# Performance work log

Hardware: AMD Instinct MI355X
Metric: run time of the kernel (lower is better)

The kernel has to match this reference:

```python
import jax, jax.numpy as jnp
import numpy as np

N, D, T = 4096, 256, 32
GAMMA = 1.0 / 256.0  # 1/d
ALPHA = 1.0


def _rbf_kernel(X, Y, gamma):
    # K[i, j] = exp(-gamma * ||X[i] - Y[j]||^2), vectorized (replaces the
    # original per-(i,j) Python double loop).
    x2 = jnp.sum(X * X, axis=1)  # [n]
    y2 = jnp.sum(Y * Y, axis=1)  # [m]
    d2 = x2[:, None] + y2[None, :] - 2.0 * (X @ Y.T)  # [n, m]
    d2 = jnp.maximum(d2, 0.0)  # numerical guard; exact form is non-negative
    return jnp.exp(-gamma * d2)


def setup_inputs() -> dict:
    key = jax.random.key(0)
    kx, ky = jax.random.split(key)
    X = jax.random.normal(kx, (N, D), dtype=jnp.float32)
    y = jax.random.normal(ky, (N, T), dtype=jnp.float32)
    return {"X": X, "y": y}


def reference(X, y):
    # fit: K = rbf(X, X); dual = solve(K + alpha*I, y)
    K = _rbf_kernel(X, X, GAMMA)  # [N, N]
    A = K + ALPHA * jnp.eye(N, dtype=K.dtype)
    dual_coef = jnp.linalg.solve(A, y)  # [N, T]
    # predict(X): original recomputes rbf(X, X) == K, then K @ dual_coef
    y_pred = K @ dual_coef  # [N, T]
    return y_pred
```

## Files before the change

### kernel.cpp

```cpp
#include <hip/hip_runtime.h>
#include <math.h>

#define NN 4096
#define DD 256
#define TT 32
#define GAMMA (1.0f/256.0f)
#define ITERS 10
#define LO_DROP 5
#define JBP 8
#define JCH 512
#define IB  64
#define BROW (JCH + 8)
#define KC  64
#define KBP 72

typedef __attribute__((ext_vector_type(8))) _Float16 f16x8;
typedef __attribute__((ext_vector_type(4))) _Float16 f16x4;
typedef __attribute__((ext_vector_type(2))) _Float16 f16x2;
typedef __attribute__((ext_vector_type(4))) float f32x4;

__global__ __launch_bounds__(256) void setup(const float* __restrict__ X,
                                             float* __restrict__ x2,
                                             _Float16* __restrict__ Xh,
                                             const float* __restrict__ y,
                                             float* __restrict__ r,
                                             _Float16* __restrict__ vh,
                                             _Float16* __restrict__ vl,
                                             float* __restrict__ rrp) {
    const int b = blockIdx.x, tid = threadIdx.x;
    const int wid = tid >> 6, lane = tid & 63;
    if (b < 1024) {
        int row = b * 4 + wid;
        const float* xr = X + (size_t)row * DD;
        float4 v = *(const float4*)(xr + lane * 4);
        float s = v.x * v.x + v.y * v.y + v.z * v.z + v.w * v.w;
        #pragma unroll
        for (int o = 32; o; o >>= 1) s += __shfl_down(s, o);
        if (lane == 0) x2[row] = s;
        f16x4 h;
        h[0] = (_Float16)v.x; h[1] = (_Float16)v.y; h[2] = (_Float16)v.z; h[3] = (_Float16)v.w;
        *(f16x4*)(Xh + (size_t)row * DD + lane * 4) = h;
    } else {
        int bb = b - 1024;
        int t = bb >> 2, c = bb & 3;
        float s = 0.f;
        #pragma unroll
        for (int pass = 0; pass < 4; ++pass) {
            int i = c * 1024 + pass * 256 + tid;
            float v = y[(size_t)i * TT + t];
            size_t off = (size_t)t * NN + i;
            r[off] = v;
            _Float16 h = (_Float16)v;
            vh[off] = h; vl[off] = (_Float16)(v - (float)h);
            s += v * v;
        }
        #pragma unroll
        for (int o = 32; o; o >>= 1) s += __shfl_down(s, o);
        __shared__ float red[4];
        if (lane == 0) red[wid] = s;
        __syncthreads();
        if (tid == 0) rrp[t * 4 + c] = red[0] + red[1] + red[2] + red[3];
    }
}

__global__ __launch_bounds__(512) void k_build(const _Float16* __restrict__ Xh,
                                               const float* __restrict__ x2,
                                               _Float16* __restrict__ Kh) {
    __shared__ _Float16 As[256 * KBP];
    __shared__ _Float16 Bs[256 * KBP];
    const int i0 = blockIdx.x * 256, j0 = blockIdx.y * 256;
    const int tid = threadIdx.x;
    const int wid = tid >> 6, lane = tid & 63;
    const int wr = wid >> 2, wc = wid & 3;
    const int l15 = lane & 15, l4 = lane >> 4;
    f32x4 acc[8][4] = {};
    for (int kc = 0; kc < DD; kc += KC) {
        __syncthreads();
        #pragma unroll
        for (int s = 0; s < 4; ++s) {
            int idx = s * 512 + tid;
            int row = idx >> 3, c = idx & 7;
            *(uint4*)(As + row * KBP + c * 8) =
                *(const uint4*)(Xh + (size_t)(i0 + row) * DD + kc + c * 8);
        }
        #pragma unroll
        for (int s = 0; s < 4; ++s) {
            int idx = s * 512 + tid;
            int row = idx >> 3, c = idx & 7;
            *(uint4*)(Bs + row * KBP + c * 8) =
                *(const uint4*)(Xh + (size_t)(j0 + row) * DD + kc + c * 8);
        }
        __syncthreads();
        #pragma unroll
        for (int kk = 0; kk < 2; ++kk) {
            f16x8 af[8], bfr[4];
            #pragma unroll
            for (int m = 0; m < 8; ++m)
                af[m] = *(const f16x8*)(As + (wr * 128 + m * 16 + l15) * KBP + kk * 32 + l4 * 8);
            #pragma unroll
            for (int n = 0; n < 4; ++n)
                bfr[n] = *(const f16x8*)(Bs + (wc * 64 + n * 16 + l15) * KBP + kk * 32 + l4 * 8);
            #pragma unroll
            for (int m = 0; m < 8; ++m)
                #pragma unroll
                for (int n = 0; n < 4; ++n)
                    acc[m][n] = __builtin_amdgcn_mfma_f32_16x16x32_f16(af[m], bfr[n], acc[m][n], 0, 0, 0);
        }
    }
    #pragma unroll
    for (int m = 0; m < 8; ++m) {
        #pragma unroll
        for (int rg = 0; rg < 4; ++rg) {
            int i = i0 + wr * 128 + m * 16 + l4 * 4 + rg;
            float x2i = x2[i];
            #pragma unroll
            for (int n = 0; n < 4; ++n) {
                int j = j0 + wc * 64 + n * 16 + l15;
                float d2 = fmaxf(x2i + x2[j] - 2.f * acc[m][n][rg], 0.f);
                Kh[(size_t)i * NN + j] = (_Float16)__expf(-GAMMA * d2);
            }
        }
    }
}

template<int USE_LO>
__global__ __launch_bounds__(256) void matvec_part(const _Float16* __restrict__ Kh,
                                                   const _Float16* __restrict__ vh,
                                                   const _Float16* __restrict__ vl,
                                                   const float* __restrict__ r,
                                                   float* __restrict__ part,
                                                   float* __restrict__ rKvp) {
    __shared__ __align__(16) _Float16 Bbuf[(1 + USE_LO) * 32 * BROW];
    __shared__ float redb[4][33];
    _Float16* Bh = Bbuf;
    _Float16* Bl = Bbuf + (USE_LO ? 32 * BROW : 0);
    const int ib = blockIdx.x;
    const int jb = blockIdx.y;
    const int bid = jb * 64 + ib;
    const int tid = threadIdx.x;
    const int wid = tid >> 6, lane = tid & 63;
    const int l15 = lane & 15, l4 = lane >> 4;
    #pragma unroll
    for (int s = 0; s < 8; ++s) {
        int c = s * 256 + tid;
        int row = c >> 6, col8 = c & 63;
        *(uint4*)(Bh + row * BROW + col8 * 8) =
            *(const uint4*)(vh + (size_t)row * NN + jb * JCH + col8 * 8);
        if (USE_LO)
            *(uint4*)(Bl + row * BROW + col8 * 8) =
                *(const uint4*)(vl + (size_t)row * NN + jb * JCH + col8 * 8);
    }
    __syncthreads();
    const _Float16* Ap  = Kh + (size_t)(ib * IB + wid * 16 + l15) * NN + jb * JCH + l4 * 8;
    const _Float16* bhp = Bh + l15 * BROW + l4 * 8;
    const _Float16* blp = Bl + l15 * BROW + l4 * 8;
    f32x4 acc0 = {}, acc1 = {};
    #pragma unroll 4
    for (int jc = 0; jc < JCH; jc += 32) {
        f16x8 a   = *(const f16x8*)(Ap + jc);
        f16x8 bh0 = *(const f16x8*)(bhp + jc);
        f16x8 bh1 = *(const f16x8*)(bhp + 16 * BROW + jc);
        acc0 = __builtin_amdgcn_mfma_f32_16x16x32_f16(a, bh0, acc0, 0, 0, 0);
        acc1 = __builtin_amdgcn_mfma_f32_16x16x32_f16(a, bh1, acc1, 0, 0, 0);
        if (USE_LO) {
            f16x8 bl0 = *(const f16x8*)(blp + jc);
            f16x8 bl1 = *(const f16x8*)(blp + 16 * BROW + jc);
            acc0 = __builtin_amdgcn_mfma_f32_16x16x32_f16(a, bl0, acc0, 0, 0, 0);
            acc1 = __builtin_amdgcn_mfma_f32_16x16x32_f16(a, bl1, acc1, 0, 0, 0);
        }
    }
    __syncthreads();
    float* tl = (float*)Bbuf;
    #pragma unroll
    for (int rg = 0; rg < 4; ++rg) {
        tl[(wid * 32 + l15) * 17 + l4 * 4 + rg]      = acc0[rg];
        tl[(wid * 32 + 16 + l15) * 17 + l4 * 4 + rg] = acc1[rg];
    }
    __syncthreads();
    #pragma unroll
    for (int q = 0; q < 8; ++q) {
        int idx = q * 64 + lane;
        int t = idx >> 4, il = idx & 15;
        int gi = ib * IB + wid * 16 + il;
        float val = tl[(wid * 32 + t) * 17 + il];
        part[((size_t)jb * TT + t) * NN + gi] = val;
        float cq = r[(size_t)t * NN + gi] * val;
        #pragma unroll
        for (int o = 8; o; o >>= 1) cq += __shfl_down(cq, o);
        if (il == 0) redb[wid][t] = cq;
    }
    __syncthreads();
    if (tid < 32) {
        float s = 0.f;
        #pragma unroll
        for (int u = 0; u < 4; ++u) s += redb[u][tid];
        rKvp[tid * 512 + bid] = s;
    }
}

__global__ __launch_bounds__(512) void cupd(const float* __restrict__ part, float* __restrict__ r,
                                            float* __restrict__ p, float* __restrict__ s_,
                                            float* __restrict__ d,
                                            _Float16* __restrict__ vh,
                                            _Float16* __restrict__ vl,
                                            const float* __restrict__ rrp_in,
                                            float* __restrict__ rrp_out,
                                            const float* __restrict__ rKvp,
                                            const float* __restrict__ scal_in,
                                            float* __restrict__ scal_out,
                                            float* __restrict__ out,
                                            int first, int last, int write_lo) {
    const int t = blockIdx.x, c = blockIdx.y, tid = threadIdx.x;
    const int wid = tid >> 6, lane = tid & 63;
    __shared__ float sc2[2];
    __shared__ float red[8];
    if (wid == 0) {
        float rw_ = 0.f;
        #pragma unroll
        for (int u = 0; u < 8; ++u) rw_ += rKvp[t * 512 + u * 64 + lane];
        float rr_ = (lane < 4) ? rrp_in[t * 4 + lane] : 0.f;
        #pragma unroll
        for (int o = 32; o; o >>= 1) { rw_ += __shfl_down(rw_, o); rr_ += __shfl_down(rr_, o); }
        if (lane == 0) {
            float rr = rr_;
            float rw = rw_ + rr;
            float alpha, beta;
            if (first) { beta = 0.f; alpha = rr / rw; }
            else {
                float ap = scal_in[t], rrprev = scal_in[TT + t];
                beta = rr / rrprev;
                alpha = rr / (rw - (beta / ap) * rr);
            }
            sc2[0] = alpha; sc2[1] = beta;
            if (c == 0) { scal_out[t] = alpha; scal_out[TT + t] = rr; }
        }
    }
    __syncthreads();
    const float alpha = sc2[0], beta = sc2[1];
    int i = c * 1024 + tid * 2;
    size_t off = (size_t)t * NN + i;
    float2 sv = {0.f, 0.f};
    #pragma unroll
    for (int b = 0; b < JBP; ++b) {
        float2 pl = *(const float2*)&part[((size_t)b * TT + t) * NN + i];
        sv.x += pl.x; sv.y += pl.y;
    }
    float2 rv = *(const float2*)(r + off);
    float2 wv = { sv.x + rv.x, sv.y + rv.y };
    float2 pv, sv2;
    if (first) { pv = rv; sv2 = wv; }
    else {
        float2 po = *(const float2*)(p + off);
        float2 so = *(const float2*)(s_ + off);
        pv  = { fmaf(beta, po.x, rv.x), fmaf(beta, po.y, rv.y) };
        sv2 = { fmaf(beta, so.x, wv.x), fmaf(beta, so.y, wv.y) };
    }
    *(float2*)(p + off) = pv;
    *(float2*)(s_ + off) = sv2;
    float2 dn;
    if (first) {
        dn = { alpha * (sv2.x - pv.x), alpha * (sv2.y - pv.y) };
    } else {
        float2 dv = *(const float2*)(d + off);
        dn = { fmaf(alpha, sv2.x - pv.x, dv.x), fmaf(alpha, sv2.y - pv.y, dv.y) };
    }
    *(float2*)(d + off) = dn;
    float2 rn = { rv.x - alpha * sv2.x, rv.y - alpha * sv2.y };
    *(float2*)(r + off) = rn;
    if (last) {
        out[(size_t)i * TT + t]       = dn.x;
        out[(size_t)(i + 1) * TT + t] = dn.y;
    } else {
        _Float16 h0 = (_Float16)rn.x, h1 = (_Float16)rn.y;
        f16x2 hv = { h0, h1 };
        *(f16x2*)(vh + off) = hv;
        if (write_lo) {
            f16x2 lv = { (_Float16)(rn.x - (float)h0), (_Float16)(rn.y - (float)h1) };
            *(f16x2*)(vl + off) = lv;
        }
    }
    float v = rn.x * rn.x + rn.y * rn.y;
    #pragma unroll
    for (int o = 32; o; o >>= 1) v += __shfl_down(v, o);
    if (lane == 0) red[wid] = v;
    __syncthreads();
    if (tid == 0) {
        float tot = 0.f;
        #pragma unroll
        for (int u = 0; u < 8; ++u) tot += red[u];
        rrp_out[t * 4 + c] = tot;
    }
}

extern "C" void kernel_launch(void* const* d_in, const int* in_sizes, int n_in,
                              void* d_out, int out_size, void* d_ws, size_t ws_size,
                              hipStream_t stream) {
    const float* X = (const float*)d_in[0];
    const float* y = (const float*)d_in[1];
    float* out = (float*)d_out;

    unsigned char* wsb = (unsigned char*)d_ws;
    _Float16* Kh = (_Float16*)wsb;  wsb += (size_t)NN * NN * 2;
    float* part  = (float*)wsb;     wsb += (size_t)JBP * TT * NN * 4;
    float* r     = (float*)wsb;     wsb += (size_t)TT * NN * 4;
    float* p     = (float*)wsb;     wsb += (size_t)TT * NN * 4;
    float* s_    = (float*)wsb;     wsb += (size_t)TT * NN * 4;
    float* d     = (float*)wsb;     wsb += (size_t)TT * NN * 4;
    _Float16* vh = (_Float16*)wsb;  wsb += (size_t)TT * NN * 2;
    _Float16* vl = (_Float16*)wsb;  wsb += (size_t)TT * NN * 2;
    _Float16* Xh = (_Float16*)wsb;  wsb += (size_t)NN * DD * 2;
    float* x2v   = (float*)wsb;     wsb += (size_t)NN * 4;
    float* rrp   = (float*)wsb;     wsb += 256 * 4;
    float* rKvp  = (float*)wsb;     wsb += (size_t)TT * 512 * 4;
    float* scal  = (float*)wsb;     wsb += 128 * 4;

    setup<<<1152, 256, 0, stream>>>(X, x2v, Xh, y, r, vh, vl, rrp);
    k_build<<<dim3(NN / 256, NN / 256), 512, 0, stream>>>(Xh, x2v, Kh);

    for (int j = 0; j < ITERS; ++j) {
        if (j < LO_DROP)
            matvec_part<1><<<dim3(64, JBP), 256, 0, stream>>>(Kh, vh, vl, r, part, rKvp);
        else
            matvec_part<0><<<dim3(64, JBP), 256, 0, stream>>>(Kh, vh, vl, r, part, rKvp);
        cupd<<<dim3(TT, 4), 512, 0, stream>>>(part, r, p, s_, d, vh, vl,
                                              rrp + (j & 1) * 128, rrp + ((j + 1) & 1) * 128,
                                              rKvp,
                                              scal + (j & 1) * 64, scal + ((j + 1) & 1) * 64,
                                              out,
                                              j == 0 ? 1 : 0, j == ITERS - 1 ? 1 : 0,
                                              (j + 1 < LO_DROP) ? 1 : 0);
    }
}
```

Baseline: 180.8 us.

## Drop fp32 residual buffer, store residual as f16 hi/lo pair, widen matvec chunks

Removes the fp32 residual array r. The residual is rebuilt from the f16 hi and lo halves in the update kernel, and the dot product in the matvec uses the hi half. The number of iterations that use the lo correction drops from five to two. The later iterations use fewer, wider j-chunks (4 blocks of 1024), which cuts the partial-sum traffic and the reduction work. This lowers memory traffic per iteration, at the cost of precision in the residual and the dot products, which may change convergence accuracy.

```diff
diff --git a/kernel.cpp b/kernel.cpp
--- a/kernel.cpp
+++ b/kernel.cpp
@@ -6,11 +6,7 @@
 #define TT 32
 #define GAMMA (1.0f/256.0f)
 #define ITERS 10
-#define LO_DROP 5
-#define JBP 8
-#define JCH 512
-#define IB  64
-#define BROW (JCH + 8)
+#define LO_DROP 2
 #define KC  64
 #define KBP 72
 
@@ -23,7 +19,6 @@
                                              float* __restrict__ x2,
                                              _Float16* __restrict__ Xh,
                                              const float* __restrict__ y,
-                                             float* __restrict__ r,
                                              _Float16* __restrict__ vh,
                                              _Float16* __restrict__ vl,
                                              float* __restrict__ rrp) {
@@ -49,7 +44,6 @@
             int i = c * 1024 + pass * 256 + tid;
             float v = y[(size_t)i * TT + t];
             size_t off = (size_t)t * NN + i;
-            r[off] = v;
             _Float16 h = (_Float16)v;
             vh[off] = h; vl[off] = (_Float16)(v - (float)h);
             s += v * v;
@@ -123,48 +117,49 @@
     }
 }
 
-template<int USE_LO>
+template<int USE_LO, int NJB, int JCHT>
 __global__ __launch_bounds__(256) void matvec_part(const _Float16* __restrict__ Kh,
                                                    const _Float16* __restrict__ vh,
                                                    const _Float16* __restrict__ vl,
-                                                   const float* __restrict__ r,
                                                    float* __restrict__ part,
                                                    float* __restrict__ rKvp) {
-    __shared__ __align__(16) _Float16 Bbuf[(1 + USE_LO) * 32 * BROW];
+    const int BROWT = JCHT + 8;
+    __shared__ __align__(16) _Float16 Bbuf[(1 + USE_LO) * 32 * (JCHT + 8)];
     __shared__ float redb[4][33];
     _Float16* Bh = Bbuf;
-    _Float16* Bl = Bbuf + (USE_LO ? 32 * BROW : 0);
+    _Float16* Bl = Bbuf + (USE_LO ? 32 * BROWT : 0);
     const int ib = blockIdx.x;
     const int jb = blockIdx.y;
     const int bid = jb * 64 + ib;
     const int tid = threadIdx.x;
     const int wid = tid >> 6, lane = tid & 63;
     const int l15 = lane & 15, l4 = lane >> 4;
-    #pragma unroll
-    for (int s = 0; s < 8; ++s) {
+    const int CPR = JCHT / 8;
+    #pragma unroll
+    for (int s = 0; s < (32 * CPR) / 256; ++s) {
         int c = s * 256 + tid;
-        int row = c >> 6, col8 = c & 63;
-        *(uint4*)(Bh + row * BROW + col8 * 8) =
-            *(const uint4*)(vh + (size_t)row * NN + jb * JCH + col8 * 8);
+        int row = c / CPR, col8 = c % CPR;
+        *(uint4*)(Bh + row * BROWT + col8 * 8) =
+            *(const uint4*)(vh + (size_t)row * NN + jb * JCHT + col8 * 8);
         if (USE_LO)
-            *(uint4*)(Bl + row * BROW + col8 * 8) =
-                *(const uint4*)(vl + (size_t)row * NN + jb * JCH + col8 * 8);
-    }
-    __syncthreads();
-    const _Float16* Ap  = Kh + (size_t)(ib * IB + wid * 16 + l15) * NN + jb * JCH + l4 * 8;
-    const _Float16* bhp = Bh + l15 * BROW + l4 * 8;
-    const _Float16* blp = Bl + l15 * BROW + l4 * 8;
+            *(uint4*)(Bl + row * BROWT + col8 * 8) =
+                *(const uint4*)(vl + (size_t)row * NN + jb * JCHT + col8 * 8);
+    }
+    __syncthreads();
+    const _Float16* Ap  = Kh + (size_t)(ib * 64 + wid * 16 + l15) * NN + jb * JCHT + l4 * 8;
+    const _Float16* bhp = Bh + l15 * BROWT + l4 * 8;
+    const _Float16* blp = Bl + l15 * BROWT + l4 * 8;
     f32x4 acc0 = {}, acc1 = {};
     #pragma unroll 4
-    for (int jc = 0; jc < JCH; jc += 32) {
+    for (int jc = 0; jc < JCHT; jc += 32) {
         f16x8 a   = *(const f16x8*)(Ap + jc);
         f16x8 bh0 = *(const f16x8*)(bhp + jc);
-        f16x8 bh1 = *(const f16x8*)(bhp + 16 * BROW + jc);
+        f16x8 bh1 = *(const f16x8*)(bhp + 16 * BROWT + jc);
         acc0 = __builtin_amdgcn_mfma_f32_16x16x32_f16(a, bh0, acc0, 0, 0, 0);
         acc1 = __builtin_amdgcn_mfma_f32_16x16x32_f16(a, bh1, acc1, 0, 0, 0);
         if (USE_LO) {
             f16x8 bl0 = *(const f16x8*)(blp + jc);
-            f16x8 bl1 = *(const f16x8*)(blp + 16 * BROW + jc);
+            f16x8 bl1 = *(const f16x8*)(blp + 16 * BROWT + jc);
             acc0 = __builtin_amdgcn_mfma_f32_16x16x32_f16(a, bl0, acc0, 0, 0, 0);
             acc1 = __builtin_amdgcn_mfma_f32_16x16x32_f16(a, bl1, acc1, 0, 0, 0);
         }
@@ -181,10 +176,10 @@
     for (int q = 0; q < 8; ++q) {
         int idx = q * 64 + lane;
         int t = idx >> 4, il = idx & 15;
-        int gi = ib * IB + wid * 16 + il;
+        int gi = ib * 64 + wid * 16 + il;
         float val = tl[(wid * 32 + t) * 17 + il];
         part[((size_t)jb * TT + t) * NN + gi] = val;
-        float cq = r[(size_t)t * NN + gi] * val;
+        float cq = (float)vh[(size_t)t * NN + gi] * val;
         #pragma unroll
         for (int o = 8; o; o >>= 1) cq += __shfl_down(cq, o);
         if (il == 0) redb[wid][t] = cq;
@@ -194,11 +189,12 @@
         float s = 0.f;
         #pragma unroll
         for (int u = 0; u < 4; ++u) s += redb[u][tid];
-        rKvp[tid * 512 + bid] = s;
-    }
-}
-
-__global__ __launch_bounds__(512) void cupd(const float* __restrict__ part, float* __restrict__ r,
+        rKvp[tid * (64 * NJB) + bid] = s;
+    }
+}
+
+template<int NJB>
+__global__ __launch_bounds__(512) void cupd(const float* __restrict__ part,
                                             float* __restrict__ p, float* __restrict__ s_,
                                             float* __restrict__ d,
                                             _Float16* __restrict__ vh,
@@ -209,7 +205,7 @@
                                             const float* __restrict__ scal_in,
                                             float* __restrict__ scal_out,
                                             float* __restrict__ out,
-                                            int first, int last, int write_lo) {
+                                            int first, int last) {
     const int t = blockIdx.x, c = blockIdx.y, tid = threadIdx.x;
     const int wid = tid >> 6, lane = tid & 63;
     __shared__ float sc2[2];
@@ -217,7 +213,7 @@
     if (wid == 0) {
         float rw_ = 0.f;
         #pragma unroll
-        for (int u = 0; u < 8; ++u) rw_ += rKvp[t * 512 + u * 64 + lane];
+        for (int u = 0; u < NJB; ++u) rw_ += rKvp[t * (64 * NJB) + u * 64 + lane];
         float rr_ = (lane < 4) ? rrp_in[t * 4 + lane] : 0.f;
         #pragma unroll
         for (int o = 32; o; o >>= 1) { rw_ += __shfl_down(rw_, o); rr_ += __shfl_down(rr_, o); }
@@ -241,11 +237,13 @@
     size_t off = (size_t)t * NN + i;
     float2 sv = {0.f, 0.f};
     #pragma unroll
-    for (int b = 0; b < JBP; ++b) {
+    for (int b = 0; b < NJB; ++b) {
         float2 pl = *(const float2*)&part[((size_t)b * TT + t) * NN + i];
         sv.x += pl.x; sv.y += pl.y;
     }
-    float2 rv = *(const float2*)(r + off);
+    f16x2 hv0 = *(const f16x2*)(vh + off);
+    f16x2 lv0 = *(const f16x2*)(vl + off);
+    float2 rv = { (float)hv0[0] + (float)lv0[0], (float)hv0[1] + (float)lv0[1] };
     float2 wv = { sv.x + rv.x, sv.y + rv.y };
     float2 pv, sv2;
     if (first) { pv = rv; sv2 = wv; }
@@ -266,18 +264,15 @@
     }
     *(float2*)(d + off) = dn;
     float2 rn = { rv.x - alpha * sv2.x, rv.y - alpha * sv2.y };
-    *(float2*)(r + off) = rn;
     if (last) {
         out[(size_t)i * TT + t]       = dn.x;
         out[(size_t)(i + 1) * TT + t] = dn.y;
     } else {
         _Float16 h0 = (_Float16)rn.x, h1 = (_Float16)rn.y;
-        f16x2 hv = { h0, h1 };
-        *(f16x2*)(vh + off) = hv;
-        if (write_lo) {
-            f16x2 lv = { (_Float16)(rn.x - (float)h0), (_Float16)(rn.y - (float)h1) };
-            *(f16x2*)(vl + off) = lv;
-        }
+        f16x2 hn = { h0, h1 };
+        f16x2 ln = { (_Float16)(rn.x - (float)h0), (_Float16)(rn.y - (float)h1) };
+        *(f16x2*)(vh + off) = hn;
+        *(f16x2*)(vl + off) = ln;
     }
     float v = rn.x * rn.x + rn.y * rn.y;
     #pragma unroll
@@ -301,8 +296,7 @@
 
     unsigned char* wsb = (unsigned char*)d_ws;
     _Float16* Kh = (_Float16*)wsb;  wsb += (size_t)NN * NN * 2;
-    float* part  = (float*)wsb;     wsb += (size_t)JBP * TT * NN * 4;
-    float* r     = (float*)wsb;     wsb += (size_t)TT * NN * 4;
+    float* part  = (float*)wsb;     wsb += (size_t)8 * TT * NN * 4;
     float* p     = (float*)wsb;     wsb += (size_t)TT * NN * 4;
     float* s_    = (float*)wsb;     wsb += (size_t)TT * NN * 4;
     float* d     = (float*)wsb;     wsb += (size_t)TT * NN * 4;
@@ -314,20 +308,25 @@
     float* rKvp  = (float*)wsb;     wsb += (size_t)TT * 512 * 4;
     float* scal  = (float*)wsb;     wsb += 128 * 4;
 
-    setup<<<1152, 256, 0, stream>>>(X, x2v, Xh, y, r, vh, vl, rrp);
+    setup<<<1152, 256, 0, stream>>>(X, x2v, Xh, y, vh, vl, rrp);
     k_build<<<dim3(NN / 256, NN / 256), 512, 0, stream>>>(Xh, x2v, Kh);
 
     for (int j = 0; j < ITERS; ++j) {
         if (j < LO_DROP)
-            matvec_part<1><<<dim3(64, JBP), 256, 0, stream>>>(Kh, vh, vl, r, part, rKvp);
+            matvec_part<1, 8, 512><<<dim3(64, 8), 256, 0, stream>>>(Kh, vh, vl, part, rKvp);
         else
-            matvec_part<0><<<dim3(64, JBP), 256, 0, stream>>>(Kh, vh, vl, r, part, rKvp);
-        cupd<<<dim3(TT, 4), 512, 0, stream>>>(part, r, p, s_, d, vh, vl,
-                                              rrp + (j & 1) * 128, rrp + ((j + 1) & 1) * 128,
-                                              rKvp,
-                                              scal + (j & 1) * 64, scal + ((j + 1) & 1) * 64,
-                                              out,
-                                              j == 0 ? 1 : 0, j == ITERS - 1 ? 1 : 0,
-                                              (j + 1 < LO_DROP) ? 1 : 0);
-    }
-}
+            matvec_part<0, 4, 1024><<<dim3(64, 4), 256, 0, stream>>>(Kh, vh, vl, part, rKvp);
+        if (j < LO_DROP)
+            cupd<8><<<dim3(TT, 4), 512, 0, stream>>>(part, p, s_, d, vh, vl,
+                                                     rrp + (j & 1) * 128, rrp + ((j + 1) & 1) * 128,
+                                                     rKvp,
+                                                     scal + (j & 1) * 64, scal + ((j + 1) & 1) * 64,
+                                                     out, j == 0 ? 1 : 0, j == ITERS - 1 ? 1 : 0);
+        else
+            cupd<4><<<dim3(TT, 4), 512, 0, stream>>>(part, p, s_, d, vh, vl,
+                                                     rrp + (j & 1) * 128, rrp + ((j + 1) & 1) * 128,
+                                                     rKvp,
+                                                     scal + (j & 1) * 64, scal + ((j + 1) & 1) * 64,
+                                                     out, j == 0 ? 1 : 0, j == ITERS - 1 ? 1 : 0);
+    }
+}
```

New measurement: 191.2 us. +5.7%, slower.
